# Optimization experiments

Hardware: AMD Instinct MI355X
Metric: run time of the kernel (lower is better)

Reference implementation:

```python
import jax, jax.numpy as jnp
import numpy as np

jax.config.update("jax_enable_x64", True)

POOL = np.array([4.0, 4.0, 4.0], dtype=np.float32)  # pool_size
N, E, D, B = 400_000, 3_200_000, 64, 16


def setup_inputs() -> dict:
    key = jax.random.key(0)
    k1, k2, k3, k4 = jax.random.split(key, 4)
    x = jax.random.normal(k1, (N, D), dtype=jnp.float32)
    pos = jax.random.uniform(k2, (N, 3), dtype=jnp.float32) * 128.0
    batch = jnp.sort(jax.random.randint(k3, (N,), 0, B)).astype(jnp.int64)
    edge_index = jax.random.randint(k4, (E, 2), 0, N).astype(jnp.int64)
    return {"x": x, "pos": pos, "edge_index": edge_index, "batch": batch}


def _voxel_key(pos, batch):
    # torch.div(pos, pool, rounding_mode='floor').long()
    qpos = jnp.floor(pos / jnp.asarray(POOL)).astype(jnp.int64)  # [N,3]
    strides = [int(qpos[:, i].max()) + 1 for i in range(3)]
    k = batch.astype(jnp.int64)
    for i in range(3):
        k = k * strides[i] + qpos[:, i]  # linearized (batch, qx, qy, qz) key
    return k, strides


def reference(x, pos, edge_index, batch):
    keyv, s = _voxel_key(pos, batch)
    ukey, inv = jnp.unique(keyv, return_inverse=True)  # unique voxel keys
    M = int(ukey.shape[0])
    new_batch = ukey // (s[0] * s[1] * s[2])  # recover batch id from key prefix

    # average_positions=True: scatter-mean of pos (include_self=False == pure mean)
    counts = jax.ops.segment_sum(jnp.ones((pos.shape[0],), pos.dtype), inv, num_segments=M)
    pos_mean = jax.ops.segment_sum(pos, inv, num_segments=M) / counts[:, None]

    # scatter-reduce amax of features (every segment non-empty by construction)
    pooled_x = jax.ops.segment_max(x, inv, num_segments=M)

    # remap edges, drop self-loops, dedup, append self-loops for all M nodes
    ei = inv[edge_index]  # [E,2]
    mask = ei[:, 0] != ei[:, 1]
    enc = ei[:, 0].astype(jnp.int64) * M + ei[:, 1].astype(jnp.int64)
    uenc = jnp.unique(enc[mask])
    ei_dedup = jnp.stack([uenc // M, uenc % M], axis=1)
    ar = jnp.arange(M, dtype=ei_dedup.dtype)
    loops = jnp.stack([ar, ar], axis=1)
    ei_out = jnp.concatenate([ei_dedup, loops], axis=0)

    return pooled_x, pos_mean, ei_out, new_batch
```

## Files before the change

### kernel.cpp

```cpp
#include <hip/hip_runtime.h>


#define KSP 524288
#define SCAN_BLOCK 256
#define SCAN_ITEMS 16
#define SCAN_CHUNK 4096
#define NCHUNK (KSP / SCAN_CHUNK)
#define NPART 2048
#define PSHIFT 8
#define PB 256
#define SCAP2 4096
#define NCOARSE 64
#define CSHIFT 13
#define CMASK 8191u
#define PS_ITERS 16


__global__ void k_keys(const float* __restrict__ pos, const int* __restrict__ batch,
                       unsigned* __restrict__ key, unsigned* __restrict__ cnt, int N) {
  int i = blockIdx.x * blockDim.x + threadIdx.x;
  if (i >= N) return;
  unsigned q0 = (unsigned)(int)floorf(pos[3 * i + 0] * 0.25f);
  unsigned q1 = (unsigned)(int)floorf(pos[3 * i + 1] * 0.25f);
  unsigned q2 = (unsigned)(int)floorf(pos[3 * i + 2] * 0.25f);
  unsigned k = ((((((unsigned)batch[i] << 5) | q0) << 5) | q1) << 5) | q2;
  key[i] = k;
  atomicAdd(&cnt[k], 1u);
}

__global__ void scanA2(const unsigned* __restrict__ in, unsigned* __restrict__ outRank,
                       unsigned* __restrict__ outStart, unsigned* __restrict__ chunkP,
                       unsigned* __restrict__ chunkC, int n) {
  __shared__ unsigned ldsP[SCAN_BLOCK];
  __shared__ unsigned ldsC[SCAN_BLOCK];
  int tbase = blockIdx.x * SCAN_CHUNK + threadIdx.x * SCAN_ITEMS;
  unsigned valsP[SCAN_ITEMS], valsC[SCAN_ITEMS];
  unsigned sp = 0, sc = 0;
  for (int i = 0; i < SCAN_ITEMS; ++i) {
    unsigned v = 0;
    int idx = tbase + i;
    if (idx < n) v = in[idx];
    valsP[i] = sp; valsC[i] = sc;
    sp += v ? 1u : 0u;
    sc += v;
  }
  ldsP[threadIdx.x] = sp; ldsC[threadIdx.x] = sc;
  __syncthreads();
  for (int off = 1; off < SCAN_BLOCK; off <<= 1) {
    unsigned tp = (threadIdx.x >= (unsigned)off) ? ldsP[threadIdx.x - off] : 0u;
    unsigned tc = (threadIdx.x >= (unsigned)off) ? ldsC[threadIdx.x - off] : 0u;
    __syncthreads();
    ldsP[threadIdx.x] += tp; ldsC[threadIdx.x] += tc;
    __syncthreads();
  }
  unsigned exP = ldsP[threadIdx.x] - sp;
  unsigned exC = ldsC[threadIdx.x] - sc;
  for (int i = 0; i < SCAN_ITEMS; ++i) {
    int idx = tbase + i;
    if (idx < n) { outRank[idx] = exP + valsP[i]; outStart[idx] = exC + valsC[i]; }
  }
  if (threadIdx.x == SCAN_BLOCK - 1) {
    chunkP[blockIdx.x] = ldsP[SCAN_BLOCK - 1];
    chunkC[blockIdx.x] = ldsC[SCAN_BLOCK - 1];
  }
}

__global__ void scanB2(unsigned* chunkP, unsigned* chunkC, unsigned* mDst) {
  __shared__ unsigned lp[NCHUNK];
  __shared__ unsigned lc[NCHUNK];
  unsigned t = threadIdx.x;
  unsigned vp = chunkP[t], vc = chunkC[t];
  lp[t] = vp; lc[t] = vc;
  __syncthreads();
  for (int off = 1; off < NCHUNK; off <<= 1) {
    unsigned xp = (t >= (unsigned)off) ? lp[t - off] : 0u;
    unsigned xc = (t >= (unsigned)off) ? lc[t - off] : 0u;
    __syncthreads();
    lp[t] += xp; lc[t] += xc;
    __syncthreads();
  }
  chunkP[t] = lp[t] - vp;
  chunkC[t] = lc[t] - vc;
  if (t == NCHUNK - 1 && mDst) *mDst = lp[NCHUNK - 1];
}

__global__ void scanC2(unsigned* __restrict__ rank, unsigned* __restrict__ ptStart,
                       const unsigned* __restrict__ chunkP, const unsigned* __restrict__ chunkC,
                       int n) {
  int idx = blockIdx.x * blockDim.x + threadIdx.x;
  if (idx >= n) return;
  int ch = idx / SCAN_CHUNK;
  rank[idx] += chunkP[ch];
  ptStart[idx] += chunkC[ch];
}

__global__ void k_scanP(const unsigned* __restrict__ in, unsigned* __restrict__ outStart,
                        unsigned* __restrict__ outCursor, unsigned* __restrict__ ccur,
                        unsigned* __restrict__ totalDst) {
  __shared__ unsigned lds[1024];
  unsigned t = threadIdx.x;
  unsigned a = in[2 * t], b = in[2 * t + 1];
  unsigned sum = a + b;
  lds[t] = sum;
  __syncthreads();
  for (int off = 1; off < 1024; off <<= 1) {
    unsigned x = (t >= (unsigned)off) ? lds[t - off] : 0u;
    __syncthreads();
    lds[t] += x;
    __syncthreads();
  }
  unsigned excl = lds[t] - sum;
  outStart[2 * t] = excl;
  outStart[2 * t + 1] = excl + a;
  if (outCursor) { outCursor[2 * t] = excl; outCursor[2 * t + 1] = excl + a; }
  if (ccur && (t & 15u) == 0) ccur[t >> 4] = excl;
  if (t == 1023) {
    outStart[NPART] = lds[1023];
    if (totalDst) *totalDst = lds[1023];
  }
}

__global__ void k_ukey(const unsigned* __restrict__ cnt, const unsigned* __restrict__ rank,
                       const unsigned* __restrict__ ptStart, const unsigned* __restrict__ hdr,
                       unsigned* __restrict__ ukeyArr, unsigned* __restrict__ cStart, int N) {
  int k = blockIdx.x * blockDim.x + threadIdx.x;
  if (k >= KSP) return;
  if (cnt[k]) {
    unsigned r = rank[k];
    ukeyArr[r] = (unsigned)k;
    cStart[r] = ptStart[k];
  }
  if (k == 0) cStart[hdr[3]] = (unsigned)N;
}

__global__ void k_scatter(const unsigned* __restrict__ key, const unsigned* __restrict__ rank,
                          unsigned* __restrict__ inv, unsigned* __restrict__ ptStart,
                          unsigned* __restrict__ ptOrder, int N) {
  int i = blockIdx.x * blockDim.x + threadIdx.x;
  if (i >= N) return;
  unsigned k = key[i];
  inv[i] = rank[k];
  unsigned posn = atomicAdd(&ptStart[k], 1u);
  ptOrder[posn] = (unsigned)i;
}

__global__ void __launch_bounds__(256) k_pool(const float4* __restrict__ x4,
                                              const float* __restrict__ pos,
                                              const unsigned* __restrict__ ptOrder,
                                              const unsigned* __restrict__ cStart,
                                              const unsigned* __restrict__ hdr,
                                              float* __restrict__ out) {
  unsigned gtid = blockIdx.x * blockDim.x + threadIdx.x;
  unsigned m = gtid >> 3;
  unsigned l = gtid & 7u;
  unsigned M = hdr[3];
  if (m >= M) return;
  unsigned start = cStart[m];
  unsigned n = cStart[m + 1] - start;
  const float NI = -__builtin_huge_valf();
  float4 a0 = make_float4(NI, NI, NI, NI);
  float4 a1 = a0;
  float psum = 0.0f;
  for (unsigned j = 0; j < n; ++j) {
    unsigned p = ptOrder[start + j];
    float4 v0 = x4[p * 16u + l];
    float4 v1 = x4[p * 16u + 8u + l];
    a0.x = fmaxf(a0.x, v0.x); a0.y = fmaxf(a0.y, v0.y);
    a0.z = fmaxf(a0.z, v0.z); a0.w = fmaxf(a0.w, v0.w);
    a1.x = fmaxf(a1.x, v1.x); a1.y = fmaxf(a1.y, v1.y);
    a1.z = fmaxf(a1.z, v1.z); a1.w = fmaxf(a1.w, v1.w);
    if (l < 3) psum += pos[3u * p + l];
  }
  float4* o4 = (float4*)out;
  o4[m * 16u + l] = a0;
  o4[m * 16u + 8u + l] = a1;
  if (l < 3) {
    unsigned long long O1 = 64ull * M;
    out[O1 + 3ull * m + l] = psum / (float)n;
  }
}

__global__ void __launch_bounds__(256) k_ehist(const int2* __restrict__ ei,
                                               const unsigned* __restrict__ inv,
                                               unsigned* __restrict__ partCnt, int E) {
  __shared__ unsigned h[NPART];
  for (int i = threadIdx.x; i < NPART; i += 256) h[i] = 0;
  __syncthreads();
  int lo = blockIdx.x * (256 * PS_ITERS);
  unsigned av[PS_ITERS];
#pragma unroll
  for (int it = 0; it < PS_ITERS; ++it) {
    int e = lo + threadIdx.x + it * 256;
    av[it] = (e < E) ? (unsigned)ei[e].x : 0xFFFFFFFFu;
  }
#pragma unroll
  for (int it = 0; it < PS_ITERS; ++it) {
    if (av[it] != 0xFFFFFFFFu) av[it] = inv[av[it]];
  }
#pragma unroll
  for (int it = 0; it < PS_ITERS; ++it) {
    if (av[it] != 0xFFFFFFFFu) atomicAdd(&h[av[it] >> PSHIFT], 1u);
  }
  __syncthreads();
  for (int i = threadIdx.x; i < NPART; i += 256) {
    unsigned v = h[i];
    if (v) atomicAdd(&partCnt[i], v);
  }
}

__global__ void __launch_bounds__(256) k_pscat1(const int2* __restrict__ ei,
                                                const unsigned* __restrict__ inv,
                                                unsigned* __restrict__ ccur,
                                                unsigned* __restrict__ stage1, int E) {
  __shared__ unsigned h[NCOARSE];
  if (threadIdx.x < NCOARSE) h[threadIdx.x] = 0;
  __syncthreads();
  int lo = blockIdx.x * (256 * PS_ITERS);
  unsigned long long codes[PS_ITERS];
#pragma unroll
  for (int it = 0; it < PS_ITERS; ++it) {
    codes[it] = ~0ull;
    int e = lo + threadIdx.x + it * 256;
    if (e < E) {
      int2 pr = ei[e];
      unsigned a = inv[pr.x], b = inv[pr.y];
      codes[it] = ((unsigned long long)a << 19) | b;
      atomicAdd(&h[a >> CSHIFT], 1u);
    }
  }
  __syncthreads();
  if (threadIdx.x < NCOARSE) {
    unsigned v = h[threadIdx.x];
    h[threadIdx.x] = v ? atomicAdd(&ccur[threadIdx.x], v) : 0u;
  }
  __syncthreads();
#pragma unroll
  for (int it = 0; it < PS_ITERS; ++it) {
    unsigned long long code = codes[it];
    if (code != ~0ull) {
      unsigned a = (unsigned)(code >> 19);
      unsigned off = atomicAdd(&h[a >> CSHIFT], 1u);
      stage1[off] = ((a & CMASK) << 19) | ((unsigned)code & 0x7FFFFu);
    }
  }
}

__global__ void __launch_bounds__(256) k_pscat2(const unsigned* __restrict__ stage1,
                                                const unsigned* __restrict__ partStart,
                                                unsigned* __restrict__ partCursor,
                                                unsigned* __restrict__ pStage) {
  __shared__ unsigned h[NPART];
  __shared__ unsigned cbL[NCOARSE + 1];
  __shared__ unsigned c0s;
  for (int i = threadIdx.x; i < NPART; i += 256) h[i] = 0;
  if (threadIdx.x <= NCOARSE) cbL[threadIdx.x] = partStart[threadIdx.x << 5];
  __syncthreads();
  unsigned base = blockIdx.x * (256u * PS_ITERS);
  unsigned validE = cbL[NCOARSE];
  if (base >= validE) return;
  if (threadIdx.x == 0) {
    unsigned c = 0;
    while (cbL[c + 1] <= base) ++c;
    c0s = c;
  }
  __syncthreads();
  unsigned codes[PS_ITERS], prt[PS_ITERS];
  unsigned c = c0s;
#pragma unroll
  for (int it = 0; it < PS_ITERS; ++it) {
    prt[it] = 0xFFFFFFFFu;
    unsigned g = base + threadIdx.x + it * 256u;
    if (g < validE) {
      while (cbL[c + 1] <= g) ++c;
      unsigned code = stage1[g];
      codes[it] = code;
      unsigned part = (c << 5) | (code >> 27);
      prt[it] = part;
      atomicAdd(&h[part], 1u);
    }
  }
  __syncthreads();
  for (int i = threadIdx.x; i < NPART; i += 256) {
    unsigned v = h[i];
    h[i] = v ? atomicAdd(&partCursor[i], v) : 0u;
  }
  __syncthreads();
#pragma unroll
  for (int it = 0; it < PS_ITERS; ++it) {
    if (prt[it] != 0xFFFFFFFFu) {
      unsigned off = atomicAdd(&h[prt[it]], 1u);
      pStage[off] = codes[it] & 0x07FFFFFFu;
    }
  }
}

__global__ void __launch_bounds__(256) k_bucket(unsigned* __restrict__ pStage,
                                                const unsigned* __restrict__ partStart,
                                                unsigned* __restrict__ partDistinct) {
  __shared__ unsigned dstL[SCAP2];
  __shared__ unsigned h[PB];
  __shared__ unsigned bbase[PB + 1];
  __shared__ unsigned stmp[256];
  unsigned p = blockIdx.x;
  unsigned s = partStart[p];
  unsigned c = partStart[p + 1] - s;
  unsigned t = threadIdx.x;
  unsigned pb = p << PSHIFT;
  h[t] = 0;
  __syncthreads();
  if (c <= SCAP2) {
    const unsigned* src = pStage + s;
    for (unsigned i = t; i < c; i += 256) atomicAdd(&h[src[i] >> 19], 1u);
    __syncthreads();
    {
      unsigned v = h[t];
      stmp[t] = v;
      __syncthreads();
      for (int off = 1; off < 256; off <<= 1) {
        unsigned x = (t >= (unsigned)off) ? stmp[t - off] : 0u;
        __syncthreads(); stmp[t] += x; __syncthreads();
      }
      bbase[t] = stmp[t] - v;
      if (t == 255) bbase[PB] = stmp[255];
    }
    __syncthreads();
    h[t] = bbase[t];
    __syncthreads();
    for (unsigned i = t; i < c; i += 256) {
      unsigned code = src[i];
      unsigned off = atomicAdd(&h[code >> 19], 1u);
      dstL[off] = code;
    }
    __syncthreads();
    unsigned L = (c + 255) >> 8;
    unsigned vv[16], rr[16];
#pragma unroll
    for (unsigned k = 0; k < 16; ++k) {
      unsigned i = t * L + k;
      if (k < L && i < c) {
        unsigned v = dstL[i];
        unsigned b = v >> 19;
        unsigned blo = bbase[b], bhi = bbase[b + 1];
        unsigned r = blo;
        for (unsigned j = blo; j < bhi; ++j) {
          unsigned u = dstL[j];
          r += (u < v) || (u == v && j < i);
        }
        vv[k] = v; rr[k] = r;
      }
    }
    __syncthreads();
#pragma unroll
    for (unsigned k = 0; k < 16; ++k) {
      unsigned i = t * L + k;
      if (k < L && i < c) dstL[rr[k]] = vv[k];
    }
    __syncthreads();
    unsigned flm = 0, localSum = 0;
#pragma unroll
    for (unsigned k = 0; k < 16; ++k) {
      unsigned i = t * L + k;
      if (k < L && i < c) {
        unsigned v = dstL[i];
        unsigned pv = dstL[i - (i > 0 ? 1u : 0u)];
        unsigned notself = ((v & 0x7FFFFu) != (pb | (v >> 19))) ? 1u : 0u;
        unsigned f = (((i == 0) | (pv != v)) ? 1u : 0u) & notself;
        flm |= f << k;
        localSum += f;
      }
    }
    stmp[t] = localSum;
    __syncthreads();
    for (int off = 1; off < 256; off <<= 1) {
      unsigned x = (t >= (unsigned)off) ? stmp[t - off] : 0u;
      __syncthreads(); stmp[t] += x; __syncthreads();
    }
    unsigned pos = stmp[t] - localSum;
#pragma unroll
    for (unsigned k = 0; k < 16; ++k) {
      unsigned i = t * L + k;
      if (k < L && i < c && ((flm >> k) & 1u)) {
        pStage[s + pos] = dstL[i];
        ++pos;
      }
    }
    if (t == 255) partDistinct[p] = stmp[255];
  } else if (t == 0) {
    unsigned* a = pStage + s;
    for (unsigned i = 1; i < c; ++i) {
      unsigned v = a[i];
      long long j = (long long)i - 1;
      while (j >= 0 && a[j] > v) { a[j + 1] = a[j]; --j; }
      a[j + 1] = v;
    }
    unsigned d = 0, prev = 0xFFFFFFFFu;
    for (unsigned i = 0; i < c; ++i) {
      unsigned v = a[i];
      if ((i == 0 || v != prev) && ((v & 0x7FFFFu) != (pb | (v >> 19)))) { a[d] = v; ++d; }
      prev = v;
    }
    partDistinct[p] = d;
  }
}

__global__ void __launch_bounds__(256) k_ewriteP(const unsigned* __restrict__ pStage,
                                                 const unsigned* __restrict__ partStart,
                                                 const unsigned* __restrict__ partOut,
                                                 const unsigned* __restrict__ hdr,
                                                 float* __restrict__ out) {
  unsigned p = blockIdx.x;
  unsigned s = partStart[p];
  unsigned rbase = partOut[p];
  unsigned d = partOut[p + 1] - rbase;
  unsigned M = hdr[3];
  unsigned long long O2 = 67ull * M;
  unsigned pbase = p << PSHIFT;
  for (unsigned j = threadIdx.x; j < d; j += 256) {
    unsigned code = pStage[s + j];
    unsigned long long row = (unsigned long long)rbase + j;
    out[O2 + 2 * row + 0] = (float)(pbase | (code >> 19));
    out[O2 + 2 * row + 1] = (float)(code & 0x7FFFFu);
  }
}

__global__ void k_final(const unsigned* __restrict__ ukeyArr, const unsigned* __restrict__ hdr,
                        float* __restrict__ out) {
  unsigned m = blockIdx.x * blockDim.x + threadIdx.x;
  unsigned M = hdr[3];
  if (m >= M) return;
  unsigned Ed = hdr[5];
  unsigned long long O2 = 67ull * M;
  unsigned long long row = (unsigned long long)Ed + m;
  float fm = (float)m;
  out[O2 + 2 * row + 0] = fm;
  out[O2 + 2 * row + 1] = fm;
  unsigned long long O3 = O2 + 2ull * (Ed + M);
  out[O3 + m] = (float)(ukeyArr[m] >> 15);
}

extern "C" void kernel_launch(void* const* d_in, const int* in_sizes, int n_in,
                              void* d_out, int out_size, void* d_ws, size_t ws_size,
                              hipStream_t stream) {
  const float* x = (const float*)d_in[0];
  const float* pos = (const float*)d_in[1];
  const int* ei = (const int*)d_in[2];
  const int* batch = (const int*)d_in[3];
  float* out = (float*)d_out;
  int N = in_sizes[3];
  int E = in_sizes[2] / 2;

  unsigned* ws = (unsigned*)d_ws;
  unsigned* hdr          = ws;
  unsigned* cnt          = ws + 64;
  unsigned* partCnt      = cnt + KSP;
  unsigned* partDistinct = partCnt + NPART;
  unsigned* rank         = partDistinct + NPART;
  unsigned* ukeyArr      = rank + KSP;
  unsigned* cStart       = ukeyArr + KSP;
  unsigned* partStart    = cStart + KSP + 2;
  unsigned* partCursor   = partStart + NPART + 2;
  unsigned* partOut      = partCursor + NPART;
  unsigned* chunkP       = partOut + NPART + 2;
  unsigned* chunkC       = chunkP + 1024;
  unsigned* ccur         = chunkC + 1024;
  unsigned* key          = ccur + 66;
  unsigned* inv          = key + N;
  unsigned* pS32         = inv + ((N + 1) & ~1);
  unsigned* pStage       = pS32;
  unsigned* stage1       = pS32 + E;
  unsigned* ptStart  = pS32;
  unsigned* ptOrder  = pS32 + KSP;

  hipMemsetAsync(ws, 0, (size_t)(64 + KSP + 2 * NPART) * 4, stream);

  const int B = 256;
  int gN = (N + B - 1) / B;
  int gK = (KSP + B - 1) / B;
  int gP = (int)(((long long)N * 8 + B - 1) / B);
  int ebS = (E + 256 * PS_ITERS - 1) / (256 * PS_ITERS);

  k_keys<<<gN, B, 0, stream>>>(pos, batch, key, cnt, N);

  scanA2<<<NCHUNK, SCAN_BLOCK, 0, stream>>>(cnt, rank, ptStart, chunkP, chunkC, KSP);
  scanB2<<<1, NCHUNK, 0, stream>>>(chunkP, chunkC, &hdr[3]);
  scanC2<<<gK, B, 0, stream>>>(rank, ptStart, chunkP, chunkC, KSP);

  k_ukey<<<gK, B, 0, stream>>>(cnt, rank, ptStart, hdr, ukeyArr, cStart, N);
  k_scatter<<<gN, B, 0, stream>>>(key, rank, inv, ptStart, ptOrder, N);
  k_pool<<<gP, B, 0, stream>>>((const float4*)x, pos, ptOrder, cStart, hdr, out);

  const int2* ei2 = (const int2*)ei;
  k_ehist<<<ebS, 256, 0, stream>>>(ei2, inv, partCnt, E);
  k_scanP<<<1, 1024, 0, stream>>>(partCnt, partStart, partCursor, ccur, &hdr[4]);
  k_pscat1<<<ebS, 256, 0, stream>>>(ei2, inv, ccur, stage1, E);
  k_pscat2<<<ebS, 256, 0, stream>>>(stage1, partStart, partCursor, pStage);
  k_bucket<<<NPART, 256, 0, stream>>>(pStage, partStart, partDistinct);
  k_scanP<<<1, 1024, 0, stream>>>(partDistinct, partOut, nullptr, nullptr, &hdr[5]);
  k_ewriteP<<<NPART, 256, 0, stream>>>(pStage, partStart, partOut, hdr, out);
  k_final<<<gK, B, 0, stream>>>(ukeyArr, hdr, out);

  (void)n_in; (void)ws_size;
}
```

Baseline: 430.5 us.

## Fuse ukey into scan, batch scatter loads, stage edge codes, merge final writes

Folds the unique-key and cluster-start writes into the scan fixup kernel, so one launch and one pass over the counts go away. The scatter kernel now handles eight points per thread so the key and rank gathers overlap. The edge-histogram kernel now remaps both endpoints once and stores 64-bit codes to a staging buffer. The later partition scatter reads that buffer instead of gathering through inv a second time. The edge-write and final kernels are merged into one launch, trading extra staging-buffer traffic and workspace for fewer random gathers and launches.

```diff
diff --git a/kernel.cpp b/kernel.cpp
--- a/kernel.cpp
+++ b/kernel.cpp
@@ -14,6 +14,7 @@
 #define CSHIFT 13
 #define CMASK 8191u
 #define PS_ITERS 16
+#define SC_ITERS 8
 
 
 __global__ void k_keys(const float* __restrict__ pos, const int* __restrict__ batch,
@@ -86,12 +87,21 @@
 
 __global__ void scanC2(unsigned* __restrict__ rank, unsigned* __restrict__ ptStart,
                        const unsigned* __restrict__ chunkP, const unsigned* __restrict__ chunkC,
-                       int n) {
+                       const unsigned* __restrict__ cnt, const unsigned* __restrict__ hdr,
+                       unsigned* __restrict__ ukeyArr, unsigned* __restrict__ cStart,
+                       int n, int N) {
   int idx = blockIdx.x * blockDim.x + threadIdx.x;
   if (idx >= n) return;
   int ch = idx / SCAN_CHUNK;
-  rank[idx] += chunkP[ch];
-  ptStart[idx] += chunkC[ch];
+  unsigned r = rank[idx] + chunkP[ch];
+  unsigned s = ptStart[idx] + chunkC[ch];
+  rank[idx] = r;
+  ptStart[idx] = s;
+  if (cnt[idx]) {
+    ukeyArr[r] = (unsigned)idx;
+    cStart[r] = s;
+  }
+  if (idx == 0) cStart[hdr[3]] = (unsigned)N;
 }
 
 __global__ void k_scanP(const unsigned* __restrict__ in, unsigned* __restrict__ outStart,
@@ -120,28 +130,31 @@
   }
 }
 
-__global__ void k_ukey(const unsigned* __restrict__ cnt, const unsigned* __restrict__ rank,
-                       const unsigned* __restrict__ ptStart, const unsigned* __restrict__ hdr,
-                       unsigned* __restrict__ ukeyArr, unsigned* __restrict__ cStart, int N) {
-  int k = blockIdx.x * blockDim.x + threadIdx.x;
-  if (k >= KSP) return;
-  if (cnt[k]) {
-    unsigned r = rank[k];
-    ukeyArr[r] = (unsigned)k;
-    cStart[r] = ptStart[k];
-  }
-  if (k == 0) cStart[hdr[3]] = (unsigned)N;
-}
-
-__global__ void k_scatter(const unsigned* __restrict__ key, const unsigned* __restrict__ rank,
-                          unsigned* __restrict__ inv, unsigned* __restrict__ ptStart,
-                          unsigned* __restrict__ ptOrder, int N) {
-  int i = blockIdx.x * blockDim.x + threadIdx.x;
-  if (i >= N) return;
-  unsigned k = key[i];
-  inv[i] = rank[k];
-  unsigned posn = atomicAdd(&ptStart[k], 1u);
-  ptOrder[posn] = (unsigned)i;
+__global__ void __launch_bounds__(256) k_scatter(const unsigned* __restrict__ key,
+                                                 const unsigned* __restrict__ rank,
+                                                 unsigned* __restrict__ inv,
+                                                 unsigned* __restrict__ ptStart,
+                                                 unsigned* __restrict__ ptOrder, int N) {
+  int lo = blockIdx.x * (256 * SC_ITERS);
+  unsigned kk[SC_ITERS], rv[SC_ITERS];
+#pragma unroll
+  for (int it = 0; it < SC_ITERS; ++it) {
+    int e = lo + threadIdx.x + it * 256;
+    kk[it] = (e < N) ? key[e] : 0xFFFFFFFFu;
+  }
+#pragma unroll
+  for (int it = 0; it < SC_ITERS; ++it) {
+    if (kk[it] != 0xFFFFFFFFu) rv[it] = rank[kk[it]];
+  }
+#pragma unroll
+  for (int it = 0; it < SC_ITERS; ++it) {
+    if (kk[it] != 0xFFFFFFFFu) {
+      int e = lo + threadIdx.x + it * 256;
+      inv[e] = rv[it];
+      unsigned posn = atomicAdd(&ptStart[kk[it]], 1u);
+      ptOrder[posn] = (unsigned)e;
+    }
+  }
 }
 
 __global__ void __launch_bounds__(256) k_pool(const float4* __restrict__ x4,
@@ -182,24 +195,30 @@
 
 __global__ void __launch_bounds__(256) k_ehist(const int2* __restrict__ ei,
                                                const unsigned* __restrict__ inv,
-                                               unsigned* __restrict__ partCnt, int E) {
+                                               unsigned* __restrict__ partCnt,
+                                               unsigned long long* __restrict__ stage0, int E) {
   __shared__ unsigned h[NPART];
   for (int i = threadIdx.x; i < NPART; i += 256) h[i] = 0;
   __syncthreads();
   int lo = blockIdx.x * (256 * PS_ITERS);
-  unsigned av[PS_ITERS];
+  unsigned av[PS_ITERS], bv[PS_ITERS];
 #pragma unroll
   for (int it = 0; it < PS_ITERS; ++it) {
     int e = lo + threadIdx.x + it * 256;
-    av[it] = (e < E) ? (unsigned)ei[e].x : 0xFFFFFFFFu;
-  }
-#pragma unroll
-  for (int it = 0; it < PS_ITERS; ++it) {
-    if (av[it] != 0xFFFFFFFFu) av[it] = inv[av[it]];
-  }
-#pragma unroll
-  for (int it = 0; it < PS_ITERS; ++it) {
-    if (av[it] != 0xFFFFFFFFu) atomicAdd(&h[av[it] >> PSHIFT], 1u);
+    if (e < E) { int2 pr = ei[e]; av[it] = (unsigned)pr.x; bv[it] = (unsigned)pr.y; }
+    else av[it] = 0xFFFFFFFFu;
+  }
+#pragma unroll
+  for (int it = 0; it < PS_ITERS; ++it) {
+    if (av[it] != 0xFFFFFFFFu) { av[it] = inv[av[it]]; bv[it] = inv[bv[it]]; }
+  }
+#pragma unroll
+  for (int it = 0; it < PS_ITERS; ++it) {
+    if (av[it] != 0xFFFFFFFFu) {
+      int e = lo + threadIdx.x + it * 256;
+      stage0[e] = ((unsigned long long)av[it] << 19) | bv[it];
+      atomicAdd(&h[av[it] >> PSHIFT], 1u);
+    }
   }
   __syncthreads();
   for (int i = threadIdx.x; i < NPART; i += 256) {
@@ -208,8 +227,7 @@
   }
 }
 
-__global__ void __launch_bounds__(256) k_pscat1(const int2* __restrict__ ei,
-                                                const unsigned* __restrict__ inv,
+__global__ void __launch_bounds__(256) k_pscat1(const unsigned long long* __restrict__ stage0,
                                                 unsigned* __restrict__ ccur,
                                                 unsigned* __restrict__ stage1, int E) {
   __shared__ unsigned h[NCOARSE];
@@ -219,12 +237,10 @@
   unsigned long long codes[PS_ITERS];
 #pragma unroll
   for (int it = 0; it < PS_ITERS; ++it) {
-    codes[it] = ~0ull;
     int e = lo + threadIdx.x + it * 256;
-    if (e < E) {
-      int2 pr = ei[e];
-      unsigned a = inv[pr.x], b = inv[pr.y];
-      codes[it] = ((unsigned long long)a << 19) | b;
+    codes[it] = (e < E) ? stage0[e] : ~0ull;
+    if (codes[it] != ~0ull) {
+      unsigned a = (unsigned)(codes[it] >> 19);
       atomicAdd(&h[a >> CSHIFT], 1u);
     }
   }
@@ -403,39 +419,37 @@
   }
 }
 
-__global__ void __launch_bounds__(256) k_ewriteP(const unsigned* __restrict__ pStage,
-                                                 const unsigned* __restrict__ partStart,
-                                                 const unsigned* __restrict__ partOut,
-                                                 const unsigned* __restrict__ hdr,
-                                                 float* __restrict__ out) {
-  unsigned p = blockIdx.x;
-  unsigned s = partStart[p];
-  unsigned rbase = partOut[p];
-  unsigned d = partOut[p + 1] - rbase;
+__global__ void __launch_bounds__(256) k_ewrite(const unsigned* __restrict__ pStage,
+                                                const unsigned* __restrict__ partStart,
+                                                const unsigned* __restrict__ partOut,
+                                                const unsigned* __restrict__ ukeyArr,
+                                                const unsigned* __restrict__ hdr,
+                                                float* __restrict__ out) {
   unsigned M = hdr[3];
   unsigned long long O2 = 67ull * M;
-  unsigned pbase = p << PSHIFT;
-  for (unsigned j = threadIdx.x; j < d; j += 256) {
-    unsigned code = pStage[s + j];
-    unsigned long long row = (unsigned long long)rbase + j;
-    out[O2 + 2 * row + 0] = (float)(pbase | (code >> 19));
-    out[O2 + 2 * row + 1] = (float)(code & 0x7FFFFu);
-  }
-}
-
-__global__ void k_final(const unsigned* __restrict__ ukeyArr, const unsigned* __restrict__ hdr,
-                        float* __restrict__ out) {
-  unsigned m = blockIdx.x * blockDim.x + threadIdx.x;
-  unsigned M = hdr[3];
-  if (m >= M) return;
-  unsigned Ed = hdr[5];
-  unsigned long long O2 = 67ull * M;
-  unsigned long long row = (unsigned long long)Ed + m;
-  float fm = (float)m;
-  out[O2 + 2 * row + 0] = fm;
-  out[O2 + 2 * row + 1] = fm;
-  unsigned long long O3 = O2 + 2ull * (Ed + M);
-  out[O3 + m] = (float)(ukeyArr[m] >> 15);
+  if (blockIdx.x < NPART) {
+    unsigned p = blockIdx.x;
+    unsigned s = partStart[p];
+    unsigned rbase = partOut[p];
+    unsigned d = partOut[p + 1] - rbase;
+    unsigned pbase = p << PSHIFT;
+    for (unsigned j = threadIdx.x; j < d; j += 256) {
+      unsigned code = pStage[s + j];
+      unsigned long long row = (unsigned long long)rbase + j;
+      out[O2 + 2 * row + 0] = (float)(pbase | (code >> 19));
+      out[O2 + 2 * row + 1] = (float)(code & 0x7FFFFu);
+    }
+  } else {
+    unsigned m = (blockIdx.x - NPART) * 256 + threadIdx.x;
+    if (m >= M) return;
+    unsigned Ed = hdr[5];
+    unsigned long long row = (unsigned long long)Ed + m;
+    float fm = (float)m;
+    out[O2 + 2 * row + 0] = fm;
+    out[O2 + 2 * row + 1] = fm;
+    unsigned long long O3 = O2 + 2ull * (Ed + M);
+    out[O3 + m] = (float)(ukeyArr[m] >> 15);
+  }
 }
 
 extern "C" void kernel_launch(void* const* d_in, const int* in_sizes, int n_in,
@@ -466,10 +480,11 @@
   unsigned* key          = ccur + 66;
   unsigned* inv          = key + N;
   unsigned* pS32         = inv + ((N + 1) & ~1);
-  unsigned* pStage       = pS32;
-  unsigned* stage1       = pS32 + E;
   unsigned* ptStart  = pS32;
   unsigned* ptOrder  = pS32 + KSP;
+  unsigned long long* stage0 = (unsigned long long*)pS32;
+  unsigned* pStage   = pS32;
+  unsigned* stage1   = pS32 + 2 * (size_t)E;
 
   hipMemsetAsync(ws, 0, (size_t)(64 + KSP + 2 * NPART) * 4, stream);
 
@@ -477,27 +492,27 @@
   int gN = (N + B - 1) / B;
   int gK = (KSP + B - 1) / B;
   int gP = (int)(((long long)N * 8 + B - 1) / B);
+  int gS = (N + B * SC_ITERS - 1) / (B * SC_ITERS);
   int ebS = (E + 256 * PS_ITERS - 1) / (256 * PS_ITERS);
 
   k_keys<<<gN, B, 0, stream>>>(pos, batch, key, cnt, N);
 
   scanA2<<<NCHUNK, SCAN_BLOCK, 0, stream>>>(cnt, rank, ptStart, chunkP, chunkC, KSP);
   scanB2<<<1, NCHUNK, 0, stream>>>(chunkP, chunkC, &hdr[3]);
-  scanC2<<<gK, B, 0, stream>>>(rank, ptStart, chunkP, chunkC, KSP);
-
-  k_ukey<<<gK, B, 0, stream>>>(cnt, rank, ptStart, hdr, ukeyArr, cStart, N);
-  k_scatter<<<gN, B, 0, stream>>>(key, rank, inv, ptStart, ptOrder, N);
+  scanC2<<<gK, B, 0, stream>>>(rank, ptStart, chunkP, chunkC, cnt, hdr, ukeyArr, cStart,
+                               KSP, N);
+
+  k_scatter<<<gS, B, 0, stream>>>(key, rank, inv, ptStart, ptOrder, N);
   k_pool<<<gP, B, 0, stream>>>((const float4*)x, pos, ptOrder, cStart, hdr, out);
 
   const int2* ei2 = (const int2*)ei;
-  k_ehist<<<ebS, 256, 0, stream>>>(ei2, inv, partCnt, E);
+  k_ehist<<<ebS, 256, 0, stream>>>(ei2, inv, partCnt, stage0, E);
   k_scanP<<<1, 1024, 0, stream>>>(partCnt, partStart, partCursor, ccur, &hdr[4]);
-  k_pscat1<<<ebS, 256, 0, stream>>>(ei2, inv, ccur, stage1, E);
+  k_pscat1<<<ebS, 256, 0, stream>>>(stage0, ccur, stage1, E);
   k_pscat2<<<ebS, 256, 0, stream>>>(stage1, partStart, partCursor, pStage);
   k_bucket<<<NPART, 256, 0, stream>>>(pStage, partStart, partDistinct);
   k_scanP<<<1, 1024, 0, stream>>>(partDistinct, partOut, nullptr, nullptr, &hdr[5]);
-  k_ewriteP<<<NPART, 256, 0, stream>>>(pStage, partStart, partOut, hdr, out);
-  k_final<<<gK, B, 0, stream>>>(ukeyArr, hdr, out);
+  k_ewrite<<<NPART + gK, 256, 0, stream>>>(pStage, partStart, partOut, ukeyArr, hdr, out);
 
   (void)n_in; (void)ws_size;
 }
```

Measured after the change: 427.1 us. About the same (-0.8%).
